# Kernel tuning notes

Measured on AMD Instinct MI355X. Metric: run time of the kernel, lower is better.

The kernel has to match this reference:

```python
import jax, jax.numpy as jnp
import numpy as np

B, S, NX, NH = 2, 2048, 1024, 16
HD = NX // NH  # head dim = 64

def setup_inputs() -> dict:
    key = jax.random.key(0)
    k1, k2, k3 = jax.random.split(key, 3)
    return {
        "x": jax.random.normal(k1, (B, S, NX), dtype=jnp.float32),
        "c_attn_w": jax.random.normal(k2, (NX, 3 * NX), dtype=jnp.float32) * 0.02,
        "c_attn_b": jnp.zeros((3 * NX,), dtype=jnp.float32),
        "c_proj_w": jax.random.normal(k3, (NX, NX), dtype=jnp.float32) * 0.02,
        "c_proj_b": jnp.zeros((NX,), dtype=jnp.float32),
    }

def reference(x, c_attn_w, c_attn_b, c_proj_w, c_proj_b):
    b, s, nx = x.shape
    # fused QKV projection (Conv1D == affine on last dim)
    qkv = x @ c_attn_w + c_attn_b                      # [b, s, 3*nx]
    q, k, v = jnp.split(qkv, 3, axis=-1)
    # split heads -> [b, h, s, d]
    q = q.reshape(b, s, NH, HD).transpose(0, 2, 1, 3)
    k = k.reshape(b, s, NH, HD).transpose(0, 2, 1, 3)
    v = v.reshape(b, s, NH, HD).transpose(0, 2, 1, 3)
    # scaled scores with causal mask (masked_fill -1e10, matching original)
    w = jnp.einsum("bhqd,bhkd->bhqk", q, k) / jnp.sqrt(jnp.float32(HD))
    causal = jnp.tril(jnp.ones((s, s), dtype=bool))    # [s, s]
    w = jnp.where(causal[None, None, :, :], w, jnp.float32(-1e10))
    w = jax.nn.softmax(w, axis=-1)
    a = jnp.einsum("bhqk,bhkd->bhqd", w, v)            # [b, h, s, d]
    # merge heads
    a = a.transpose(0, 2, 1, 3).reshape(b, s, nx)
    # output projection (dropout is identity in eval)
    return a @ c_proj_w + c_proj_b
```

## Files before the change

kernel.cpp:

```cpp
#include <hip/hip_runtime.h>
#include <cstdint>

typedef unsigned short u16;
typedef unsigned int u32;
typedef float f32x4 __attribute__((ext_vector_type(4)));
typedef __bf16 bf16x8 __attribute__((ext_vector_type(8)));
typedef __bf16 bf16x4 __attribute__((ext_vector_type(4)));
typedef u16 u16x8 __attribute__((ext_vector_type(8)));

#define B_ 2
#define S_ 2048
#define NX_ 1024
#define NH_ 16
#define HD_ 64
#define T3_ 3072
#define M_ 4096
#define SCL 0.18033688011112042f

__device__ __forceinline__ u16 bfbits(float f) {
    __bf16 h = (__bf16)f;
    return __builtin_bit_cast(u16, h);
}

__device__ __forceinline__ void gload_lds16(const void* g, void* l) {
    auto gp = reinterpret_cast<const __attribute__((address_space(1))) u32*>(
        reinterpret_cast<uintptr_t>(g));
    auto lp = reinterpret_cast<__attribute__((address_space(3))) u32*>(
        reinterpret_cast<uintptr_t>(l));
    __builtin_amdgcn_global_load_lds(gp, lp, 16, 0, 0);
}

__global__ __launch_bounds__(256) void cvt_bf16_kernel(const float* __restrict__ X,
                                                       u16* __restrict__ Y) {
    int i = (blockIdx.x * 256 + threadIdx.x) * 4;
    float4 v = *reinterpret_cast<const float4*>(X + i);
    bf16x4 o;
    o[0] = (__bf16)v.x; o[1] = (__bf16)v.y; o[2] = (__bf16)v.z; o[3] = (__bf16)v.w;
    *reinterpret_cast<bf16x4*>(Y + i) = o;
}

__global__ __launch_bounds__(256) void transpose_cvt_kernel(const float* __restrict__ W,
                                                            u16* __restrict__ WT,
                                                            int K, int N) {
    __shared__ float tile[32][33];
    int nbx = N >> 5;
    int nb = (blockIdx.x % nbx) << 5;
    int kb = (blockIdx.x / nbx) << 5;
    int tx = threadIdx.x & 31, ty = threadIdx.x >> 5;
#pragma unroll
    for (int i = 0; i < 32; i += 8)
        tile[ty + i][tx] = W[(size_t)(kb + ty + i) * N + nb + tx];
    __syncthreads();
#pragma unroll
    for (int i = 0; i < 32; i += 8)
        WT[(size_t)(nb + ty + i) * K + kb + tx] = bfbits(tile[tx][ty + i]);
}

#define BM 128
#define BN 128
#define BK 64
__global__ __launch_bounds__(256) void gemm_bt_kernel(const u16* __restrict__ A,
                                                      const u16* __restrict__ Bt,
                                                      const float* __restrict__ bias,
                                                      u16* __restrict__ Cb,
                                                      float* __restrict__ Cf,
                                                      u16* __restrict__ Vt,
                                                      int vcol0,
                                                      int M, int N, int K) {
    __shared__ u16 a_lds[BM * BK];
    __shared__ u16 b_lds[BN * BK];
    int nbn = N / BN;
    int nwg = gridDim.x;
    int orig = blockIdx.x;
    int wg = (orig & 7) * (nwg >> 3) + (orig >> 3);
    int bm = wg / nbn, bn = wg % nbn;
    int t = threadIdx.x;
    int w = t >> 6, l = t & 63, lg = l >> 4, lr = l & 15;
    int wr = w >> 1, wc = w & 1;
    const u16* Abase = A + (size_t)bm * BM * K;
    const u16* Bbase = Bt + (size_t)bn * BN * K;

    f32x4 zero4 = {0.f, 0.f, 0.f, 0.f};
    f32x4 acc[4][4];
#pragma unroll
    for (int m = 0; m < 4; ++m)
#pragma unroll
        for (int n = 0; n < 4; ++n) acc[m][n] = zero4;

    int nkt = K / BK;
    for (int kt = 0; kt < nkt; ++kt) {
#pragma unroll
        for (int it = 0; it < 4; ++it) {
            int idx = it * 256 + t;
            int row = idx >> 3, ck = idx & 7;
            int ldsoff = (it * 256 + w * 64) * 8;
            gload_lds16(Abase + (size_t)row * K + kt * BK + ck * 8, a_lds + ldsoff);
            gload_lds16(Bbase + (size_t)row * K + kt * BK + ck * 8, b_lds + ldsoff);
        }
        __syncthreads();
#pragma unroll
        for (int ks = 0; ks < 2; ++ks) {
            bf16x8 af[4], bf[4];
#pragma unroll
            for (int m = 0; m < 4; ++m)
                af[m] = *reinterpret_cast<const bf16x8*>(
                    a_lds + (wr * 64 + m * 16 + lr) * BK + ks * 32 + lg * 8);
#pragma unroll
            for (int n = 0; n < 4; ++n)
                bf[n] = *reinterpret_cast<const bf16x8*>(
                    b_lds + (wc * 64 + n * 16 + lr) * BK + ks * 32 + lg * 8);
#pragma unroll
            for (int m = 0; m < 4; ++m)
#pragma unroll
                for (int n = 0; n < 4; ++n)
                    acc[m][n] = __builtin_amdgcn_mfma_f32_16x16x32_bf16(
                        af[m], bf[n], acc[m][n], 0, 0, 0);
        }
        __syncthreads();
    }
#pragma unroll
    for (int n = 0; n < 4; ++n) {
        int col0 = bn * BN + wc * 64 + n * 16;
        int col = col0 + lr;
        float bv = bias[col];
        bool isv = (Vt != nullptr) && (col0 >= vcol0);
#pragma unroll
        for (int m = 0; m < 4; ++m) {
            int row0 = bm * BM + wr * 64 + m * 16 + lg * 4;
            if (isv) {
                int nv = col - vcol0, hh = nv >> 6, dd = nv & 63;
                int bb = row0 >> 11, ss = row0 & 2047;
                bf16x4 pk;
#pragma unroll
                for (int r = 0; r < 4; ++r) pk[r] = (__bf16)(acc[m][n][r] + bv);
                *reinterpret_cast<bf16x4*>(
                    Vt + (((size_t)(bb * 16 + hh) * 64 + dd) << 11) + ss) = pk;
            } else {
#pragma unroll
                for (int r = 0; r < 4; ++r) {
                    float v = acc[m][n][r] + bv;
                    if (Cf) Cf[(size_t)(row0 + r) * N + col] = v;
                    else    Cb[(size_t)(row0 + r) * N + col] = bfbits(v);
                }
            }
        }
    }
}

__global__ __launch_bounds__(256) void attn_kernel(const u16* __restrict__ qkv,
                                                   const u16* __restrict__ Vt,
                                                   u16* __restrict__ outa) {
    __shared__ u16 k_lds[2][4096];
    __shared__ u16 v_lds[2][4096];
    __shared__ u16 p_lds[4096];

    int bid = blockIdx.x;
    int g = bid & 31;
    int j = bid >> 5;
    int j0 = j & 7, kk = j >> 3;
    int qt = (kk == 0) ? j0 : (kk == 1) ? (31 - j0) : (kk == 2) ? (8 + j0) : (23 - j0);
    int b = g >> 4, h = g & 15;
    int t = threadIdx.x, w = t >> 6, l = t & 63, lg = l >> 4, lr = l & 15;
    const u16* base = qkv + (size_t)b * S_ * T3_;
    const u16* vbase = Vt + (size_t)g * 64 * S_;
    int prow = w * 16 + lr;
    int srow = w * 8 + (l >> 3);
    int qb = qt * 64;
    int qrow = qb + w * 16 + lr;

    auto stage = [&](int kt2, int bs) {
        int kb2 = kt2 * 64;
#pragma unroll
        for (int it = 0; it < 2; ++it) {
            int row = it * 32 + srow;
            int ckg = (l & 7) ^ (row & 7);
            gload_lds16(base + (size_t)(kb2 + row) * T3_ + NX_ + h * 64 + ckg * 8,
                        &k_lds[bs][(it * 32 + w * 8) * 64]);
            gload_lds16(vbase + (size_t)row * S_ + kb2 + ckg * 8,
                        &v_lds[bs][(it * 32 + w * 8) * 64]);
        }
    };

    f32x4 zero4 = {0.f, 0.f, 0.f, 0.f};

    bf16x8 qf[2];
#pragma unroll
    for (int ks = 0; ks < 2; ++ks)
        qf[ks] = *reinterpret_cast<const bf16x8*>(
            base + (size_t)qrow * T3_ + h * 64 + ks * 32 + lg * 8);

    f32x4 oacc[4];
#pragma unroll
    for (int dc = 0; dc < 4; ++dc) oacc[dc] = zero4;
    float mrun = -1e30f, lrun = 0.f;
    int nkt = qt + 1;

    stage(0, 0);
    __syncthreads();

    for (int kt = 0; kt < nkt; ++kt) {
        int cur = kt & 1;
        if (kt + 1 < nkt) stage(kt + 1, cur ^ 1);

        f32x4 sacc[4];
#pragma unroll
        for (int kn = 0; kn < 4; ++kn) sacc[kn] = zero4;
        __builtin_amdgcn_s_setprio(1);
#pragma unroll
        for (int ks = 0; ks < 2; ++ks) {
#pragma unroll
            for (int kn = 0; kn < 4; ++kn) {
                bf16x8 kf = *reinterpret_cast<const bf16x8*>(
                    &k_lds[cur][(kn * 16 + lr) * 64 + (((ks * 4 + lg) ^ (lr & 7)) * 8)]);
                sacc[kn] = __builtin_amdgcn_mfma_f32_16x16x32_bf16(
                    kf, qf[ks], sacc[kn], 0, 0, 0);
            }
        }
        __builtin_amdgcn_s_setprio(0);

        if (kt == qt) {
            int qloc = w * 16 + lr;
#pragma unroll
            for (int kn = 0; kn < 4; ++kn)
#pragma unroll
                for (int r = 0; r < 4; ++r)
                    if (kn * 16 + lg * 4 + r > qloc) sacc[kn][r] = -1e30f;
        }

        float mx = -1e30f;
#pragma unroll
        for (int kn = 0; kn < 4; ++kn) {
            float a0 = fmaxf(sacc[kn][0], sacc[kn][1]);
            float a1 = fmaxf(sacc[kn][2], sacc[kn][3]);
            mx = fmaxf(mx, fmaxf(a0, a1));
        }
        mx = fmaxf(mx, __shfl_xor(mx, 16));
        mx = fmaxf(mx, __shfl_xor(mx, 32));

        bool noresc = __all(mx <= mrun + 8.0f);
        float mnew = noresc ? mrun : fmaxf(mrun, mx);

        float rs = 0.f;
#pragma unroll
        for (int kn = 0; kn < 4; ++kn)
#pragma unroll
            for (int r = 0; r < 4; ++r) {
                float pv = exp2f((sacc[kn][r] - mnew) * SCL);
                sacc[kn][r] = pv;
                rs += pv;
            }
        rs += __shfl_xor(rs, 16);
        rs += __shfl_xor(rs, 32);

        if (noresc) {
            lrun += rs;
        } else {
            float fsc = exp2f((mrun - mnew) * SCL);
            mrun = mnew;
            lrun = lrun * fsc + rs;
            float f0 = __shfl(fsc, lg * 4 + 0);
            float f1 = __shfl(fsc, lg * 4 + 1);
            float f2 = __shfl(fsc, lg * 4 + 2);
            float f3 = __shfl(fsc, lg * 4 + 3);
#pragma unroll
            for (int dc = 0; dc < 4; ++dc) {
                oacc[dc][0] *= f0; oacc[dc][1] *= f1;
                oacc[dc][2] *= f2; oacc[dc][3] *= f3;
            }
        }

#pragma unroll
        for (int kn = 0; kn < 4; ++kn) {
            bf16x4 pb;
            pb[0] = (__bf16)sacc[kn][0]; pb[1] = (__bf16)sacc[kn][1];
            pb[2] = (__bf16)sacc[kn][2]; pb[3] = (__bf16)sacc[kn][3];
            int byteoff = prow * 128 + (((2 * kn + (lg >> 1)) ^ (prow & 7)) * 16) + (lg & 1) * 8;
            *reinterpret_cast<bf16x4*>(reinterpret_cast<char*>(p_lds) + byteoff) = pb;
        }

        __builtin_amdgcn_s_setprio(1);
#pragma unroll
        for (int ks = 0; ks < 2; ++ks) {
            bf16x8 pf = *reinterpret_cast<const bf16x8*>(
                reinterpret_cast<char*>(p_lds) + prow * 128 + (((ks * 4 + lg) ^ (prow & 7)) * 16));
#pragma unroll
            for (int dc = 0; dc < 4; ++dc) {
                bf16x8 vf = *reinterpret_cast<const bf16x8*>(
                    &v_lds[cur][(dc * 16 + lr) * 64 + (((ks * 4 + lg) ^ (lr & 7)) * 8)]);
                oacc[dc] = __builtin_amdgcn_mfma_f32_16x16x32_bf16(
                    pf, vf, oacc[dc], 0, 0, 0);
            }
        }
        __builtin_amdgcn_s_setprio(0);
        __syncthreads();
    }

    float inv = 1.f / lrun;
    float i0 = __shfl(inv, lg * 4 + 0);
    float i1 = __shfl(inv, lg * 4 + 1);
    float i2 = __shfl(inv, lg * 4 + 2);
    float i3 = __shfl(inv, lg * 4 + 3);
    u16* ob = outa + (size_t)b * S_ * NX_;
#pragma unroll
    for (int r = 0; r < 4; ++r) {
        float ir = (r == 0) ? i0 : (r == 1) ? i1 : (r == 2) ? i2 : i3;
        int row = qb + w * 16 + lg * 4 + r;
#pragma unroll
        for (int dc = 0; dc < 4; ++dc)
            ob[(size_t)row * NX_ + h * 64 + dc * 16 + lr] = bfbits(oacc[dc][r] * ir);
    }
}

extern "C" void kernel_launch(void* const* d_in, const int* in_sizes, int n_in,
                              void* d_out, int out_size, void* d_ws, size_t ws_size,
                              hipStream_t stream) {
    const float* x        = (const float*)d_in[0];
    const float* c_attn_w = (const float*)d_in[1];
    const float* c_attn_b = (const float*)d_in[2];
    const float* c_proj_w = (const float*)d_in[3];
    const float* c_proj_b = (const float*)d_in[4];
    float* out = (float*)d_out;

    u16* xb     = (u16*)d_ws;
    u16* wqkvT  = xb + (size_t)M_ * NX_;
    u16* wprojT = wqkvT + (size_t)T3_ * NX_;
    u16* qkv    = wprojT + (size_t)NX_ * NX_;
    u16* attno  = xb;
    u16* Vtp    = (u16*)d_out;

    cvt_bf16_kernel<<<(M_ * NX_) / 1024, 256, 0, stream>>>(x, xb);
    transpose_cvt_kernel<<<(T3_ / 32) * (NX_ / 32), 256, 0, stream>>>(c_attn_w, wqkvT, NX_, T3_);
    transpose_cvt_kernel<<<(NX_ / 32) * (NX_ / 32), 256, 0, stream>>>(c_proj_w, wprojT, NX_, NX_);
    gemm_bt_kernel<<<(M_ / BM) * (T3_ / BN), 256, 0, stream>>>(
        xb, wqkvT, c_attn_b, qkv, nullptr, Vtp, 2 * NX_, M_, T3_, NX_);
    attn_kernel<<<1024, 256, 0, stream>>>(qkv, Vtp, attno);
    gemm_bt_kernel<<<(M_ / BM) * (NX_ / BN), 256, 0, stream>>>(
        attno, wprojT, c_proj_b, nullptr, out, nullptr, 0, M_, NX_, NX_);
}
```

Baseline: 127.9 us.

## Add 256x256 double-buffered swizzled GEMM kernel for QKV projection

Introduces a new 512-thread GEMM kernel with 256x256 tiles, double-buffered LDS staging via direct global-to-LDS loads, and XOR-swizzled LDS layout to avoid bank conflicts, and uses it for the QKV projection. Larger tiles raise arithmetic intensity and prefetching the next K-tile overlaps loads with MFMA work; setprio raises priority around the MFMA bursts. The trade-off is only 192 workgroups for the GPU's CUs and heavy LDS use limiting occupancy. The old kernel is simplified and kept for the output projection.

Result: no change. 129.3 us (+1.1%).

```diff
diff --git a/kernel.cpp b/kernel.cpp
--- a/kernel.cpp
+++ b/kernel.cpp
@@ -64,8 +64,6 @@
                                                       const float* __restrict__ bias,
                                                       u16* __restrict__ Cb,
                                                       float* __restrict__ Cf,
-                                                      u16* __restrict__ Vt,
-                                                      int vcol0,
                                                       int M, int N, int K) {
     __shared__ u16 a_lds[BM * BK];
     __shared__ u16 b_lds[BN * BK];
@@ -120,13 +118,112 @@
     }
 #pragma unroll
     for (int n = 0; n < 4; ++n) {
-        int col0 = bn * BN + wc * 64 + n * 16;
+        int col = bn * BN + wc * 64 + n * 16 + lr;
+        float bv = bias[col];
+#pragma unroll
+        for (int m = 0; m < 4; ++m) {
+            int row0 = bm * BM + wr * 64 + m * 16 + lg * 4;
+#pragma unroll
+            for (int r = 0; r < 4; ++r) {
+                float v = acc[m][n][r] + bv;
+                if (Cf) Cf[(size_t)(row0 + r) * N + col] = v;
+                else    Cb[(size_t)(row0 + r) * N + col] = bfbits(v);
+            }
+        }
+    }
+}
+
+__global__ __launch_bounds__(512, 2) void gemm256_bt_kernel(const u16* __restrict__ A,
+                                                            const u16* __restrict__ Bt,
+                                                            const float* __restrict__ bias,
+                                                            u16* __restrict__ Cb,
+                                                            u16* __restrict__ Vt,
+                                                            int vcol0,
+                                                            int M, int N, int K) {
+    __shared__ u16 a_lds[2][256 * 64];
+    __shared__ u16 b_lds[2][256 * 64];
+    int nbn = N / 256;
+    int nwg = gridDim.x;
+    int orig = blockIdx.x;
+    int wg = (orig & 7) * (nwg >> 3) + (orig >> 3);
+    int bm = wg / nbn, bn = wg % nbn;
+    int t = threadIdx.x;
+    int wid = t >> 6, l = t & 63, lg = l >> 4, lr = l & 15;
+    int wr = wid >> 2, wc = wid & 3;
+    const u16* Abase = A + (size_t)bm * 256 * K;
+    const u16* Bbase = Bt + (size_t)bn * 256 * K;
+
+    f32x4 acc[8][4] = {};
+
+    auto stage = [&](int kt, int bs) {
+#pragma unroll
+        for (int gld = 0; gld < 4; ++gld) {
+            int idx = gld * 512 + wid * 64 + l;
+            int row = idx >> 3, ck = idx & 7;
+            int cds = ck ^ (row & 7);
+            int ubase = (gld * 512 + wid * 64) * 8;
+            gload_lds16(Abase + (size_t)row * K + kt * 64 + cds * 8, &a_lds[bs][ubase]);
+            gload_lds16(Bbase + (size_t)row * K + kt * 64 + cds * 8, &b_lds[bs][ubase]);
+        }
+    };
+
+    stage(0, 0);
+    __syncthreads();
+
+    int nkt = K / 64;
+    for (int kt = 0; kt < nkt; ++kt) {
+        int cur = kt & 1;
+        if (kt + 1 < nkt) stage(kt + 1, cur ^ 1);
+
+#pragma unroll
+        for (int ph = 0; ph < 4; ++ph) {
+            int mh = ph >> 1, nh = ph & 1;
+            bf16x8 af[4][2], bf[2][2];
+#pragma unroll
+            for (int mm = 0; mm < 4; ++mm) {
+                int row = wr * 128 + (mh * 4 + mm) * 16 + lr;
+#pragma unroll
+                for (int ks = 0; ks < 2; ++ks) {
+                    int ck = (ks * 4 + lg) ^ (row & 7);
+                    af[mm][ks] = *reinterpret_cast<const bf16x8*>(
+                        &a_lds[cur][row * 64 + ck * 8]);
+                }
+            }
+#pragma unroll
+            for (int nn = 0; nn < 2; ++nn) {
+                int row = wc * 64 + (nh * 2 + nn) * 16 + lr;
+#pragma unroll
+                for (int ks = 0; ks < 2; ++ks) {
+                    int ck = (ks * 4 + lg) ^ (row & 7);
+                    bf[nn][ks] = *reinterpret_cast<const bf16x8*>(
+                        &b_lds[cur][row * 64 + ck * 8]);
+                }
+            }
+            __builtin_amdgcn_s_setprio(1);
+#pragma unroll
+            for (int ks = 0; ks < 2; ++ks)
+#pragma unroll
+                for (int mm = 0; mm < 4; ++mm)
+#pragma unroll
+                    for (int nn = 0; nn < 2; ++nn)
+                        acc[mh * 4 + mm][nh * 2 + nn] =
+                            __builtin_amdgcn_mfma_f32_16x16x32_bf16(
+                                af[mm][ks], bf[nn][ks],
+                                acc[mh * 4 + mm][nh * 2 + nn], 0, 0, 0);
+            __builtin_amdgcn_s_setprio(0);
+        }
+        __syncthreads();
+    }
+
+#pragma unroll
+    for (int n = 0; n < 4; ++n) {
+        int col0 = bn * 256 + wc * 64 + n * 16;
         int col = col0 + lr;
         float bv = bias[col];
         bool isv = (Vt != nullptr) && (col0 >= vcol0);
 #pragma unroll
-        for (int m = 0; m < 4; ++m) {
-            int row0 = bm * BM + wr * 64 + m * 16 + lg * 4;
+        for (int m = 0; m < 8; ++m) {
+            int row0 = bm * 256 + wr * 128 + m * 16 + lg * 4;
             if (isv) {
                 int nv = col - vcol0, hh = nv >> 6, dd = nv & 63;
                 int bb = row0 >> 11, ss = row0 & 2047;
@@ -137,11 +234,8 @@
                     Vt + (((size_t)(bb * 16 + hh) * 64 + dd) << 11) + ss) = pk;
             } else {
 #pragma unroll
-                for (int r = 0; r < 4; ++r) {
-                    float v = acc[m][n][r] + bv;
-                    if (Cf) Cf[(size_t)(row0 + r) * N + col] = v;
-                    else    Cb[(size_t)(row0 + r) * N + col] = bfbits(v);
-                }
+                for (int r = 0; r < 4; ++r)
+                    Cb[(size_t)(row0 + r) * N + col] = bfbits(acc[m][n][r] + bv);
             }
         }
     }
@@ -331,9 +425,9 @@
     cvt_bf16_kernel<<<(M_ * NX_) / 1024, 256, 0, stream>>>(x, xb);
     transpose_cvt_kernel<<<(T3_ / 32) * (NX_ / 32), 256, 0, stream>>>(c_attn_w, wqkvT, NX_, T3_);
     transpose_cvt_kernel<<<(NX_ / 32) * (NX_ / 32), 256, 0, stream>>>(c_proj_w, wprojT, NX_, NX_);
-    gemm_bt_kernel<<<(M_ / BM) * (T3_ / BN), 256, 0, stream>>>(
-        xb, wqkvT, c_attn_b, qkv, nullptr, Vtp, 2 * NX_, M_, T3_, NX_);
+    gemm256_bt_kernel<<<(M_ / 256) * (T3_ / 256), 512, 0, stream>>>(
+        xb, wqkvT, c_attn_b, qkv, Vtp, 2 * NX_, M_, T3_, NX_);
     attn_kernel<<<1024, 256, 0, stream>>>(qkv, Vtp, attno);
     gemm_bt_kernel<<<(M_ / BM) * (NX_ / BN), 256, 0, stream>>>(
-        attno, wprojT, c_proj_b, nullptr, out, nullptr, 0, M_, NX_, NX_);
-}
+        attno, wprojT, c_proj_b, nullptr, out, M_, NX_, NX_);
+}
```
